# Optimization experiments

Hardware: AMD Instinct MI355X
Metric: run time of the kernel (lower is better)

The kernel has to match this reference:

```python
import jax, jax.numpy as jnp
import numpy as np

T = 0.2


def _cdist(a, b):
    # Euclidean cdist with zero-safe sqrt (grad 0 at coincident points, like torch)
    d2 = (a * a).sum(-1)[:, None] + (b * b).sum(-1)[None, :] - 2.0 * (a @ b.T)
    d2 = jnp.maximum(d2, 0.0)
    safe = jnp.where(d2 > 0, d2, 1.0)
    return jnp.where(d2 > 0, jnp.sqrt(safe), 0.0)


def _generator(eps, W_in, b_in, W_blk, b_blk, W_out, b_out):
    x = eps @ W_in.T + b_in
    for i in range(W_blk.shape[0]):  # 4 residual MLP blocks
        x = x + jax.nn.relu(x @ W_blk[i].T + b_blk[i])
    return x @ W_out.T + b_out


def setup_inputs() -> dict:
    N, D, H = 4096, 128, 512
    key = jax.random.key(0)
    ks = jax.random.split(key, 16)

    def lin(kw, kb, fan_in, shape_w, shape_b):
        bound = 1.0 / np.sqrt(fan_in)
        W = jax.random.uniform(kw, shape_w, jnp.float32, -bound, bound)
        b = jax.random.uniform(kb, shape_b, jnp.float32, -bound, bound)
        return W, b

    W_in, b_in = lin(ks[0], ks[1], D, (H, D), (H,))
    W_blk, b_blk = lin(ks[2], ks[3], H, (4, H, H), (4, H))
    W_out, b_out = lin(ks[4], ks[5], H, (D, H), (D,))
    y_pos = jax.random.normal(ks[6], (N, D), jnp.float32)
    eps = jax.random.normal(ks[7], (N, D), jnp.float32)
    return {"y_pos": y_pos, "eps": eps, "W_in": W_in, "b_in": b_in,
            "W_blk": W_blk, "b_blk": b_blk, "W_out": W_out, "b_out": b_out}


def reference(y_pos, eps, W_in, b_in, W_blk, b_blk, W_out, b_out):
    x = _generator(eps, W_in, b_in, W_blk, b_blk, W_out, b_out)  # [N, D]
    N = y_pos.shape[0]
    dist_pos = _cdist(x, y_pos)                                   # [N, N]
    dist_neg = _cdist(x, x) + jnp.eye(x.shape[0], dtype=x.dtype) * 1e6
    A = jnp.concatenate([-dist_pos / T, -dist_neg / T], axis=-1)  # [N, 2N]
    A_row = jax.nn.softmax(A, axis=-1)
    A_col = jax.nn.softmax(A, axis=-2)
    A_soft = jnp.sqrt(A_row * A_col)
    A_pos = A_soft[:, :N]
    A_neg = A_soft[:, N:]
    s_pos = A_pos.sum(axis=1, keepdims=True)
    s_neg = A_neg.sum(axis=1, keepdims=True)
    Wpos = A_pos * s_neg
    # torch in-place: Wpos *= s_neg mutates A_pos BEFORE A_pos.sum is taken,
    # so Wneg = A_neg * (A_pos * s_neg).sum(1) = A_neg * s_pos * s_neg
    Wneg = A_neg * (s_pos * s_neg)
    V = Wpos @ y_pos - Wneg @ x                                   # drifting field
    target = jax.lax.stop_gradient(x + V)
    return jnp.mean((x - target) ** 2)
```

## Files before the change

kernel.cpp:

```cpp
#include <hip/hip_runtime.h>
#include <math.h>

#define N 4096
#define D 128
#define H 512
#define KSPLIT 4
#define SC_LOG2 7.2134752044f

typedef short bf16x8 __attribute__((ext_vector_type(8)));
typedef float f32x4 __attribute__((ext_vector_type(4)));
typedef unsigned short u16x8 __attribute__((ext_vector_type(8)));
typedef unsigned short u16;
typedef _Float16 f16;
typedef _Float16 f16x4 __attribute__((ext_vector_type(4)));

#define MFMA(a, b, c) __builtin_amdgcn_mfma_f32_16x16x32_bf16((a), (b), (c), 0, 0, 0)

__device__ __forceinline__ float fexp2(float x)
{
#if __has_builtin(__builtin_amdgcn_exp2f)
    return __builtin_amdgcn_exp2f(x);
#else
    return exp2f(x);
#endif
}

__device__ __forceinline__ float fsqrt(float x)
{
#if __has_builtin(__builtin_amdgcn_sqrtf)
    return __builtin_amdgcn_sqrtf(x);
#else
    return sqrtf(x);
#endif
}

__device__ __forceinline__ float bf2f(u16 h)
{
    return __uint_as_float(((unsigned)h) << 16);
}

__device__ __forceinline__ u16 rtn_bf16(float v)
{
    unsigned u = __float_as_uint(v);
    return (u16)((u + 0x7FFFu + ((u >> 16) & 1u)) >> 16);
}

__device__ __forceinline__ void split1(float v, u16& h, u16& l)
{
    u16 hh = rtn_bf16(v);
    float r = v - bf2f(hh);
    h = hh;
    l = rtn_bf16(r);
}

__device__ __forceinline__ void split1_trunc(float v, u16& h, u16& l)
{
    unsigned bv = __float_as_uint(v);
    unsigned hb = bv & 0xFFFF0000u;
    float r = v - __uint_as_float(hb);
    h = (u16)(hb >> 16);
    l = (u16)(__float_as_uint(r) >> 16);
}

template <int CTRL>
__device__ __forceinline__ float dppf(float x)
{
    int r = __builtin_amdgcn_update_dpp(0, __float_as_int(x), CTRL, 0xF, 0xF, true);
    return __int_as_float(r);
}

struct SplitDesc { const float* src; u16* h; int n; };
struct SplitArgs { SplitDesc d[4]; };

__global__ __launch_bounds__(256) void split_multi(SplitArgs args)
{
    SplitDesc de = args.d[blockIdx.y];
    int idx = (blockIdx.x * 256 + threadIdx.x) * 4;
    if (idx >= de.n) return;
    float4 v = *(const float4*)(de.src + idx);
    ushort4 hv;
    hv.x = rtn_bf16(v.x); hv.y = rtn_bf16(v.y);
    hv.z = rtn_bf16(v.z); hv.w = rtn_bf16(v.w);
    *(ushort4*)(de.h + idx) = hv;
}

__global__ __launch_bounds__(512) void gen_fused(
    const float* __restrict__ eps,
    const u16* __restrict__ Win, const u16* __restrict__ Wblk,
    const u16* __restrict__ Wout,
    const float* __restrict__ b_in, const float* __restrict__ b_blk,
    const float* __restrict__ b_out,
    float* __restrict__ xo, u16* __restrict__ xh)
{
    __shared__ u16 XhS[16][520], XlS[16][520];
    const int t = threadIdx.x;
    const int w = t >> 6, lane = t & 63;
    const int quad = lane >> 4, l16 = lane & 15;
    const int bm = blockIdx.x * 16;

    {
        int idx = t * 4;
        int row = idx >> 7, col = idx & 127;
        float4 v = *(const float4*)(eps + (size_t)(bm + row) * D + col);
        ushort4 hv, lv;
        split1(v.x, hv.x, lv.x); split1(v.y, hv.y, lv.y);
        split1(v.z, hv.z, lv.z); split1(v.w, hv.w, lv.w);
        *(ushort4*)&XhS[row][col] = hv;
        *(ushort4*)&XlS[row][col] = lv;
    }
    __syncthreads();

    auto layer = [&](const u16* __restrict__ W, const float* __restrict__ bias,
                     int K, bool rr) {
        const int nb = w * 64;
        f32x4 acc[4] = {};
        const int NT = K >> 5;
        bf16x8 bh[4], bn[4];
        #pragma unroll
        for (int ni = 0; ni < 4; ++ni)
            bh[ni] = *(const bf16x8*)(W + (size_t)(nb + ni * 16 + l16) * K + quad * 8);
        for (int kt = 0; kt < NT; ++kt) {
            const int kk = kt * 32 + quad * 8;
            bf16x8 af  = *(const bf16x8*)&XhS[l16][kk];
            bf16x8 alf = *(const bf16x8*)&XlS[l16][kk];
            if (kt + 1 < NT) {
                #pragma unroll
                for (int ni = 0; ni < 4; ++ni)
                    bn[ni] = *(const bf16x8*)
                        (W + (size_t)(nb + ni * 16 + l16) * K + kk + 32);
            }
            #pragma unroll
            for (int ni = 0; ni < 4; ++ni) {
                acc[ni] = MFMA(af,  bh[ni], acc[ni]);
                acc[ni] = MFMA(alf, bh[ni], acc[ni]);
            }
            if (kt + 1 < NT) {
                #pragma unroll
                for (int ni = 0; ni < 4; ++ni) bh[ni] = bn[ni];
            }
        }
        float bl4[4];
        #pragma unroll
        for (int ni = 0; ni < 4; ++ni) bl4[ni] = bias[nb + ni * 16 + l16];
        __syncthreads();
        #pragma unroll
        for (int ni = 0; ni < 4; ++ni) {
            const int col = nb + ni * 16 + l16;
            #pragma unroll
            for (int r = 0; r < 4; ++r) {
                const int row = quad * 4 + r;
                float v = acc[ni][r] + bl4[ni];
                if (rr) {
                    float prev = bf2f(XhS[row][col]) + bf2f(XlS[row][col]);
                    v = prev + fmaxf(v, 0.0f);
                }
                u16 hh, ll;
                split1_trunc(v, hh, ll);
                XhS[row][col] = hh;
                XlS[row][col] = ll;
            }
        }
        __syncthreads();
    };

    layer(Win, b_in, D, false);
    for (int i = 0; i < 4; ++i)
        layer(Wblk + (size_t)i * H * H, b_blk + i * H, H, true);

    {
        const int n0 = w * 16;
        f32x4 acc5 = {};
        const int NT = H >> 5;
        bf16x8 bh5 = *(const bf16x8*)(Wout + (size_t)(n0 + l16) * H + quad * 8);
        for (int kt = 0; kt < NT; ++kt) {
            const int kk = kt * 32 + quad * 8;
            bf16x8 af  = *(const bf16x8*)&XhS[l16][kk];
            bf16x8 alf = *(const bf16x8*)&XlS[l16][kk];
            bf16x8 bn5;
            if (kt + 1 < NT)
                bn5 = *(const bf16x8*)(Wout + (size_t)(n0 + l16) * H + kk + 32);
            acc5 = MFMA(af,  bh5, acc5);
            acc5 = MFMA(alf, bh5, acc5);
            if (kt + 1 < NT) bh5 = bn5;
        }
        const int col = n0 + l16;
        const float bl = b_out[col];
        #pragma unroll
        for (int r = 0; r < 4; ++r) {
            const int gm = bm + quad * 4 + r;
            float v = acc5[r] + bl;
            xo[(size_t)gm * D + col] = v;
            xh[(size_t)gm * D + col] = rtn_bf16(v);
        }
    }
}

__global__ __launch_bounds__(256) void rownorm(
    const float* __restrict__ X, const float* __restrict__ Y,
    float* __restrict__ nx, float* __restrict__ ny)
{
    const float* src = blockIdx.y ? Y : X;
    float* dst = blockIdx.y ? ny : nx;
    const int t = threadIdx.x;
    const int row = blockIdx.x * 64 + (t >> 2);
    const int q = t & 3;
    const float* rp = src + (size_t)row * D + q * 32;
    float s = 0.f;
    #pragma unroll
    for (int i = 0; i < 8; ++i) {
        float4 v = *(const float4*)(rp + i * 4);
        s += v.x * v.x + v.y * v.y + v.z * v.z + v.w * v.w;
    }
    s += __shfl_xor(s, 1);
    s += __shfl_xor(s, 2);
    if (q == 0) dst[row] = s;
}

__global__ __launch_bounds__(256) void transpose_rtn(
    const float* __restrict__ X, const float* __restrict__ Y,
    u16* __restrict__ Xth, u16* __restrict__ Yth)
{
    const float* src = blockIdx.z ? Y : X;
    u16* th = blockIdx.z ? Yth : Xth;
    __shared__ float tile[32][33];
    const int t = threadIdx.x;
    const int r0 = blockIdx.x * 32, c0 = blockIdx.y * 32;
    {
        int rit = t >> 3, coff = (t & 7) * 4;
        float4 v = *(const float4*)(src + (size_t)(r0 + rit) * D + c0 + coff);
        tile[rit][coff + 0] = v.x; tile[rit][coff + 1] = v.y;
        tile[rit][coff + 2] = v.z; tile[rit][coff + 3] = v.w;
    }
    __syncthreads();
    {
        int cit = t >> 3, roff = (t & 7) * 4;
        ushort4 hv;
        hv.x = rtn_bf16(tile[roff + 0][cit]);
        hv.y = rtn_bf16(tile[roff + 1][cit]);
        hv.z = rtn_bf16(tile[roff + 2][cit]);
        hv.w = rtn_bf16(tile[roff + 3][cit]);
        *(ushort4*)(th + (size_t)(c0 + cit) * N + r0 + roff) = hv;
    }
}

__global__ __launch_bounds__(256) void dist_fused(
    const u16* __restrict__ Xh, const u16* __restrict__ Yh,
    const float* __restrict__ nx, const float* __restrict__ ny,
    f16* __restrict__ Apos, f16* __restrict__ Aneg,
    float* __restrict__ prm_p, float* __restrict__ prs_p,
    float* __restrict__ pcm_p, float* __restrict__ pcs_p,
    float* __restrict__ prm_n, float* __restrict__ prs_n)
{
    const int mat = blockIdx.z;
    const u16* Bhp = mat ? Xh : Yh;
    const float* nb = mat ? nx : ny;
    f16* Out = mat ? Aneg : Apos;
    float* prm = mat ? prm_n : prm_p;
    float* prs = mat ? prs_n : prs_p;

    __shared__ u16 XhS[128][40], YhS[128][40];
    const int t = threadIdx.x;
    const int w = t >> 6, lane = t & 63;
    const int quad = lane >> 4, l16 = lane & 15;
    const int bm = blockIdx.y * 128, bn = blockIdx.x * 128;
    f32x4 acc[2][8] = {};

    for (int k0 = 0; k0 < D; k0 += 32) {
        __syncthreads();
        #pragma unroll
        for (int p = 0; p < 2; ++p) {
            int slot = t + p * 256;
            int row = slot >> 2, koff = (slot & 3) << 3;
            *(u16x8*)&XhS[row][koff] =
                *(const u16x8*)(Xh + (size_t)(bm + row) * D + k0 + koff);
        }
        #pragma unroll
        for (int p = 0; p < 2; ++p) {
            int slot = t + p * 256;
            int row = slot >> 2, koff = (slot & 3) << 3;
            int pr = ((row & 3) << 4) | ((row & 63) >> 2) | (row & 64);
            int kf = koff ^ (((pr >> 4) & 3) << 3);
            *(u16x8*)&YhS[pr][kf] =
                *(const u16x8*)(Bhp + (size_t)(bn + row) * D + k0 + koff);
        }
        __syncthreads();
        bf16x8 af[2], bhf[8];
        #pragma unroll
        for (int mi = 0; mi < 2; ++mi)
            af[mi] = *(const bf16x8*)&XhS[w * 32 + mi * 16 + l16][quad * 8];
        #pragma unroll
        for (int ni = 0; ni < 8; ++ni) {
            int nn = ni & 3, hf = ni >> 2;
            bhf[ni] = *(const bf16x8*)
                &YhS[hf * 64 + nn * 16 + l16][(quad * 8) ^ (nn << 3)];
        }
        #pragma unroll
        for (int mi = 0; mi < 2; ++mi)
            #pragma unroll
            for (int ni = 0; ni < 8; ++ni)
                acc[mi][ni] = MFMA(af[mi], bhf[ni], acc[mi][ni]);
    }
    const int jb = bn + (l16 << 2);
    const float SC2 = SC_LOG2 * SC_LOG2;
    const float c2 = -2.0f * SC2;
    const float4 n0v = *(const float4*)(nb + jb);
    const float4 n1v = *(const float4*)(nb + jb + 64);
    const float nl[8] = {n0v.x * SC2, n0v.y * SC2, n0v.z * SC2, n0v.w * SC2,
                         n1v.x * SC2, n1v.y * SC2, n1v.z * SC2, n1v.w * SC2};
    #pragma unroll
    for (int mi = 0; mi < 2; ++mi)
        #pragma unroll
        for (int r = 0; r < 4; ++r) {
            const int gm = bm + w * 32 + mi * 16 + quad * 4 + r;
            const float nxm = nx[gm] * SC2;
            f16x4 ov0, ov1;
            #pragma unroll
            for (int nn = 0; nn < 4; ++nn) {
                float s0 = fsqrt(fmaxf(
                    fmaf(acc[mi][nn][r], c2, nxm + nl[nn]), 0.f));
                float s1 = fsqrt(fmaxf(
                    fmaf(acc[mi][4 + nn][r], c2, nxm + nl[4 + nn]), 0.f));
                if (mat) {
                    if (gm == jb + nn) s0 = 5.0e6f;
                    if (gm == jb + 64 + nn) s1 = 5.0e6f;
                }
                acc[mi][nn][r] = s0;
                acc[mi][4 + nn][r] = s1;
                ov0[nn] = (f16)(-s0);
                ov1[nn] = (f16)(-s1);
            }
            *(f16x4*)(Out + (size_t)gm * N + jb) = ov0;
            *(f16x4*)(Out + (size_t)gm * N + jb + 64) = ov1;
        }
    float m[2][4];
    #pragma unroll
    for (int mi = 0; mi < 2; ++mi)
        #pragma unroll
        for (int r = 0; r < 4; ++r) {
            float v = fminf(fminf(fminf(acc[mi][0][r], acc[mi][1][r]),
                                  fminf(acc[mi][2][r], acc[mi][3][r])),
                            fminf(fminf(acc[mi][4][r], acc[mi][5][r]),
                                  fminf(acc[mi][6][r], acc[mi][7][r])));
            v = fminf(v, dppf<0xB1>(v));
            v = fminf(v, dppf<0x4E>(v));
            v = fminf(v, dppf<0x141>(v));
            v = fminf(v, dppf<0x140>(v));
            m[mi][r] = v;
        }
    float mn = fminf(fminf(fminf(m[0][0], m[0][1]), fminf(m[0][2], m[0][3])),
                     fminf(fminf(m[1][0], m[1][1]), fminf(m[1][2], m[1][3])));
    mn = fminf(mn, __shfl_xor(mn, 16));
    mn = fminf(mn, __shfl_xor(mn, 32));
    float sig[2][4] = {};
    float cs[8] = {};
    #pragma unroll
    for (int mi = 0; mi < 2; ++mi)
        #pragma unroll
        for (int ni = 0; ni < 8; ++ni) {
            float e0 = fexp2(mn - acc[mi][ni][0]);
            float e1 = fexp2(mn - acc[mi][ni][1]);
            float e2 = fexp2(mn - acc[mi][ni][2]);
            float e3 = fexp2(mn - acc[mi][ni][3]);
            sig[mi][0] += e0; sig[mi][1] += e1;
            sig[mi][2] += e2; sig[mi][3] += e3;
            cs[ni] += (e0 + e1) + (e2 + e3);
        }
    const int ct = blockIdx.x;
    #pragma unroll
    for (int mi = 0; mi < 2; ++mi)
        #pragma unroll
        for (int r = 0; r < 4; ++r) {
            float s = sig[mi][r];
            s += dppf<0xB1>(s);
            s += dppf<0x4E>(s);
            s += dppf<0x141>(s);
            s += dppf<0x140>(s);
            s *= fexp2(m[mi][r] - mn);
            if (l16 == 0) {
                int grow = bm + w * 32 + mi * 16 + quad * 4 + r;
                prm[(size_t)ct * N + grow] = -m[mi][r];
                prs[(size_t)ct * N + grow] = s;
            }
        }
    if (mat == 0) {
        const int rt = blockIdx.y * 4 + w;
        #pragma unroll
        for (int ni = 0; ni < 8; ++ni) {
            cs[ni] += __shfl_xor(cs[ni], 16);
            cs[ni] += __shfl_xor(cs[ni], 32);
        }
        if (quad == 0) {
            float4 c0 = {cs[0], cs[1], cs[2], cs[3]};
            float4 c1 = {cs[4], cs[5], cs[6], cs[7]};
            float4 m4 = {-mn, -mn, -mn, -mn};
            *(float4*)(pcs_p + (size_t)rt * N + jb) = c0;
            *(float4*)(pcs_p + (size_t)rt * N + jb + 64) = c1;
            *(float4*)(pcm_p + (size_t)rt * N + jb) = m4;
            *(float4*)(pcm_p + (size_t)rt * N + jb + 64) = m4;
        }
    }
}

__global__ __launch_bounds__(256) void stats_combine(
    const float* __restrict__ prm_p, const float* __restrict__ prs_p,
    const float* __restrict__ prm_n, const float* __restrict__ prs_n,
    const float* __restrict__ pcm_p, const float* __restrict__ pcs_p,
    float* __restrict__ m_row, float* __restrict__ isr,
    float* __restrict__ m_col, float* __restrict__ isc)
{
    __shared__ float Ms[4][64], Ss[4][64];
    const int t = threadIdx.x;
    const int g = t >> 6, l = t & 63;
    const int idx = blockIdx.x * 64 + l;

    float m = -3.0e38f, s = 0.f;
    if (idx < N) {
        const int i = idx;
        const int c0 = g * 8;
        #pragma unroll 4
        for (int c = c0; c < c0 + 8; ++c) {
            m = fmaxf(m, prm_p[(size_t)c * N + i]);
            m = fmaxf(m, prm_n[(size_t)c * N + i]);
        }
        #pragma unroll 4
        for (int c = c0; c < c0 + 8; ++c) {
            s += prs_p[(size_t)c * N + i] * fexp2(prm_p[(size_t)c * N + i] - m);
            s += prs_n[(size_t)c * N + i] * fexp2(prm_n[(size_t)c * N + i] - m);
        }
    } else {
        const int mat = (idx - N) >> 12;
        const int j = idx & (N - 1);
        const float* pm = mat ? prm_n : pcm_p;
        const float* ps = mat ? prs_n : pcs_p;
        const int cnt = mat ? 8 : 32;
        const int cb = g * cnt;
        #pragma unroll 4
        for (int c = cb; c < cb + cnt; ++c)
            m = fmaxf(m, pm[(size_t)c * N + j]);
        #pragma unroll 4
        for (int c = cb; c < cb + cnt; ++c)
            s += ps[(size_t)c * N + j] * fexp2(pm[(size_t)c * N + j] - m);
    }
    Ms[g][l] = m; Ss[g][l] = s;
    __syncthreads();
    if (g == 0) {
        float m0 = Ms[0][l], m1 = Ms[1][l], m2 = Ms[2][l], m3 = Ms[3][l];
        float mm = fmaxf(fmaxf(m0, m1), fmaxf(m2, m3));
        float ss = Ss[0][l] * fexp2(m0 - mm) + Ss[1][l] * fexp2(m1 - mm)
                 + Ss[2][l] * fexp2(m2 - mm) + Ss[3][l] * fexp2(m3 - mm);
        if (idx < N) {
            m_row[idx] = mm;
            isr[idx] = 1.0f / sqrtf(ss);
        } else {
            const int mat = (idx - N) >> 12;
            const int j = idx & (N - 1);
            m_col[mat * N + j] = mm;
            isc[mat * N + j] = 1.0f / sqrtf(ss);
        }
    }
}

__global__ __launch_bounds__(256) void pv_mfma(
    const f16* __restrict__ Apos, const f16* __restrict__ Aneg,
    const u16* __restrict__ Yth, const u16* __restrict__ Xth,
    const float* __restrict__ m_row, const float* __restrict__ isr,
    const float* __restrict__ m_col, const float* __restrict__ isc,
    float* __restrict__ u_part, float* __restrict__ w_part,
    float* __restrict__ sp_part, float* __restrict__ sn_part)
{
    const int mat = blockIdx.z;
    const f16* Am = mat ? Aneg : Apos;
    const u16* Bh = mat ? Xth : Yth;
    const float* mc = m_col + mat * N;
    const float* ic = isc + mat * N;
    float* Cp = (mat ? w_part : u_part) + (size_t)blockIdx.y * (N * D);
    float* spn = (mat ? sn_part : sp_part) + (size_t)blockIdx.y * N;

    __shared__ u16 BhS[128][72];
    __shared__ u16 PhS[64][72], PlS[64][72];
    __shared__ float mrS[64], isrS[64];

    const int t = threadIdx.x;
    const int w = t >> 6, lane = t & 63;
    const int quad = lane >> 4, l16 = lane & 15;
    const int bm = blockIdx.x * 64;
    const int jbase = blockIdx.y * (N / KSPLIT);
    const int arow = t >> 4;
    const int aj = (t & 15) << 2;

    if (t < 64) { mrS[t] = m_row[bm + t]; isrS[t] = isr[bm + t]; }

    f32x4 acc[8] = {};
    float rs[4] = {0.f, 0.f, 0.f, 0.f};

    for (int jt = 0; jt < (N / KSPLIT) / 64; ++jt) {
        const int j0 = jbase + jt * 64;
        __syncthreads();
        #pragma unroll
        for (int p = 0; p < 4; ++p) {
            int slot = t + p * 256;
            int d = slot >> 3, joff = (slot & 7) << 3;
            *(u16x8*)&BhS[d][joff] = *(const u16x8*)(Bh + (size_t)d * N + j0 + joff);
        }
        float4 mcv = *(const float4*)(mc + j0 + aj);
        float4 icv = *(const float4*)(ic + j0 + aj);
        #pragma unroll
        for (int s = 0; s < 4; ++s) {
            int row = arow + s * 16;
            f16x4 av = *(const f16x4*)(Am + (size_t)(bm + row) * N + j0 + aj);
            float mr = mrS[row], sr = isrS[row];
            float p0 = fexp2((float)av.x - 0.5f * (mr + mcv.x)) * (sr * icv.x);
            float p1 = fexp2((float)av.y - 0.5f * (mr + mcv.y)) * (sr * icv.y);
            float p2 = fexp2((float)av.z - 0.5f * (mr + mcv.z)) * (sr * icv.z);
            float p3 = fexp2((float)av.w - 0.5f * (mr + mcv.w)) * (sr * icv.w);
            rs[s] += p0 + p1 + p2 + p3;
            ushort4 hv, lv;
            split1_trunc(p0, hv.x, lv.x); split1_trunc(p1, hv.y, lv.y);
            split1_trunc(p2, hv.z, lv.z); split1_trunc(p3, hv.w, lv.w);
            *(ushort4*)&PhS[row][aj] = hv;
            *(ushort4*)&PlS[row][aj] = lv;
        }
        __syncthreads();
        #pragma unroll
        for (int ks = 0; ks < 2; ++ks) {
            const int kk = ks * 32 + quad * 8;
            bf16x8 ph = *(const bf16x8*)&PhS[w * 16 + l16][kk];
            bf16x8 pl = *(const bf16x8*)&PlS[w * 16 + l16][kk];
            #pragma unroll
            for (int ni = 0; ni < 8; ++ni) {
                bf16x8 bh = *(const bf16x8*)&BhS[ni * 16 + l16][kk];
                acc[ni] = MFMA(ph, bh, acc[ni]);
                acc[ni] = MFMA(pl, bh, acc[ni]);
            }
        }
    }
    #pragma unroll
    for (int ni = 0; ni < 8; ++ni)
        #pragma unroll
        for (int r = 0; r < 4; ++r) {
            int row = w * 16 + quad * 4 + r;
            int col = ni * 16 + l16;
            Cp[(size_t)(bm + row) * D + col] = acc[ni][r];
        }
    #pragma unroll
    for (int s = 0; s < 4; ++s) {
        float v = rs[s];
        v += __shfl_xor(v, 1); v += __shfl_xor(v, 2);
        v += __shfl_xor(v, 4); v += __shfl_xor(v, 8);
        if (l16 == 0) spn[bm + arow + s * 16] = v;
    }
}

__global__ __launch_bounds__(256) void final_reduce(const float* __restrict__ u_part,
    const float* __restrict__ w_part, const float* __restrict__ sp_part,
    const float* __restrict__ sn_part, double* __restrict__ acc_part)
{
    __shared__ float red[256];
    const int t = threadIdx.x;
    const int idx = blockIdx.x * 256 + t;
    float u = 0.f, w = 0.f;
    #pragma unroll
    for (int c = 0; c < KSPLIT; ++c) {
        u += u_part[(size_t)c * (N * D) + idx];
        w += w_part[(size_t)c * (N * D) + idx];
    }
    const int i = idx >> 7;
    float sp = 0.f, sn = 0.f;
    #pragma unroll
    for (int c = 0; c < KSPLIT; ++c) {
        sp += sp_part[(size_t)c * N + i];
        sn += sn_part[(size_t)c * N + i];
    }
    const float v = sn * u - sp * sn * w;
    red[t] = v * v; __syncthreads();
    for (int s = 128; s > 0; s >>= 1) { if (t < s) red[t] += red[t + s]; __syncthreads(); }
    if (!t) acc_part[blockIdx.x] = (double)red[0];
}

__global__ __launch_bounds__(256) void finalize(const double* __restrict__ acc_part,
                                                float* __restrict__ out)
{
    __shared__ double red[256];
    const int t = threadIdx.x;
    double s = 0.0;
    #pragma unroll
    for (int i = 0; i < 8; ++i) s += acc_part[t + i * 256];
    red[t] = s; __syncthreads();
    for (int st = 128; st > 0; st >>= 1) {
        if (t < st) red[t] += red[t + st];
        __syncthreads();
    }
    if (!t) out[0] = (float)(red[0] * (1.0 / ((double)N * (double)D)));
}

extern "C" void kernel_launch(void* const* d_in, const int* in_sizes, int n_in,
                              void* d_out, int out_size, void* d_ws, size_t ws_size,
                              hipStream_t stream)
{
    const float* y_pos = (const float*)d_in[0];
    const float* eps   = (const float*)d_in[1];
    const float* W_in  = (const float*)d_in[2];
    const float* b_in  = (const float*)d_in[3];
    const float* W_blk = (const float*)d_in[4];
    const float* b_blk = (const float*)d_in[5];
    const float* W_out = (const float*)d_in[6];
    const float* b_out = (const float*)d_in[7];
    float* out = (float*)d_out;
    (void)in_sizes; (void)n_in; (void)out_size; (void)ws_size;

    char* p = (char*)d_ws;
    auto alloc = [&](size_t bytes) {
        char* r = p;
        p += (bytes + 255) & ~(size_t)255;
        return r;
    };
    double* acc_part = (double*)alloc(2048 * 8);
    float* sp_part = (float*)alloc((size_t)KSPLIT * N * 4);
    float* sn_part = (float*)alloc((size_t)KSPLIT * N * 4);
    float* m_row  = (float*)alloc(N * 4);
    float* isr    = (float*)alloc(N * 4);
    float* m_col  = (float*)alloc(2 * N * 4);
    float* isc    = (float*)alloc(2 * N * 4);
    float* nx     = (float*)alloc(N * 4);
    float* ny     = (float*)alloc(N * 4);
    float* xo  = (float*)alloc((size_t)N * D * 4);
    u16* xh    = (u16*)alloc((size_t)N * D * 2);
    u16* xth   = (u16*)alloc((size_t)N * D * 2);
    u16* yh    = (u16*)alloc((size_t)N * D * 2);
    u16* yth   = (u16*)alloc((size_t)N * D * 2);
    char* genreg = alloc((size_t)KSPLIT * N * D * 4 * 2);
    u16* wih = (u16*)genreg;
    u16* wbh = wih + (size_t)H * D;
    u16* woh = wbh + (size_t)4 * H * H;
    float* prm_p = (float*)genreg;
    float* prs_p = prm_p + 32 * N;
    float* prm_n = prs_p + 32 * N;
    float* prs_n = prm_n + 32 * N;
    float* pcm_p = prs_n + 32 * N;
    float* pcs_p = pcm_p + 128 * N;
    float* u_part = (float*)genreg;
    float* w_part = u_part + (size_t)KSPLIT * N * D;
    f16* Apos = (f16*)alloc((size_t)N * N * 2);
    f16* Aneg = (f16*)alloc((size_t)N * N * 2);

    SplitArgs sa;
    sa.d[0] = { y_pos, yh,  N * D };
    sa.d[1] = { W_in,  wih, H * D };
    sa.d[2] = { W_blk, wbh, 4 * H * H };
    sa.d[3] = { W_out, woh, D * H };
    split_multi<<<dim3(1024, 4), 256, 0, stream>>>(sa);

    gen_fused<<<N / 16, 512, 0, stream>>>(eps, wih, wbh, woh,
                                          b_in, b_blk, b_out, xo, xh);

    rownorm<<<dim3(N / 64, 2), 256, 0, stream>>>(xo, y_pos, nx, ny);

    transpose_rtn<<<dim3(N / 32, D / 32, 2), 256, 0, stream>>>(
        xo, y_pos, xth, yth);

    dist_fused<<<dim3(N / 128, N / 128, 2), 256, 0, stream>>>(
        xh, yh, nx, ny, Apos, Aneg,
        prm_p, prs_p, pcm_p, pcs_p, prm_n, prs_n);

    stats_combine<<<192, 256, 0, stream>>>(prm_p, prs_p, prm_n, prs_n,
                                           pcm_p, pcs_p,
                                           m_row, isr, m_col, isc);

    pv_mfma<<<dim3(N / 64, KSPLIT, 2), 256, 0, stream>>>(Apos, Aneg,
        yth, xth, m_row, isr, m_col, isc, u_part, w_part, sp_part, sn_part);

    final_reduce<<<(N * D) / 256, 256, 0, stream>>>(u_part, w_part,
                                                    sp_part, sn_part, acc_part);
    finalize<<<1, 256, 0, stream>>>(acc_part, out);
}
```

Measured before the change: 228.9 us.

## Stage generator weights through LDS with double-buffered direct global-to-LDS loads

The generator MLP kernel now streams each weight K-slice into shared memory with global_load_lds double buffering, instead of each wave loading its own weight fragments into registers. The next slice is prefetched while MFMAs consume the current one, and the k loops are fully unrolled. This aims to hide global load latency and cut register pressure. In exchange it adds a block-wide barrier per k-step and about 64KB of extra LDS, which may limit occupancy.

Measured after the change: 270.9 us. 18.4% more time.

```diff
diff --git a/kernel.cpp b/kernel.cpp
--- a/kernel.cpp
+++ b/kernel.cpp
@@ -15,6 +15,9 @@
 typedef _Float16 f16x4 __attribute__((ext_vector_type(4)));
 
 #define MFMA(a, b, c) __builtin_amdgcn_mfma_f32_16x16x32_bf16((a), (b), (c), 0, 0, 0)
+
+using gvoid = const __attribute__((address_space(1))) void;
+using lvoid = __attribute__((address_space(3))) void;
 
 __device__ __forceinline__ float fexp2(float x)
 {
@@ -84,6 +87,73 @@
     *(ushort4*)(de.h + idx) = hv;
 }
 
+template <int ROWS>
+__device__ __forceinline__ void stage_w(const u16* __restrict__ W, int K, int kt,
+                                        u16* ws, int t)
+{
+    constexpr int ISS = ROWS / 128;
+    #pragma unroll
+    for (int p = 0; p < ISS; ++p) {
+        const int slot = t + p * 512;
+        const int c = slot & (ROWS - 1);
+        const int q = slot / ROWS;
+        const u16* g = W + (size_t)c * K + kt * 32 + q * 8;
+        __builtin_amdgcn_global_load_lds((gvoid*)g,
+                                         (lvoid*)(ws + (size_t)slot * 8),
+                                         16, 0, 0);
+    }
+}
+
+template <int K, bool RR>
+__device__ __forceinline__ void gen_layer(
+    u16 (&XhS)[16][520], u16 (&XlS)[16][520],
+    u16* WS0, u16* WS1,
+    const u16* __restrict__ W, const float* __restrict__ bias,
+    int w, int quad, int l16, int t)
+{
+    const int nb = w * 64;
+    constexpr int NT = K >> 5;
+    f32x4 acc[4] = {};
+    float bl4[4];
+    #pragma unroll
+    for (int ni = 0; ni < 4; ++ni) bl4[ni] = bias[nb + ni * 16 + l16];
+    #pragma unroll
+    for (int kt = 0; kt < NT; ++kt) {
+        u16* cur = (kt & 1) ? WS1 : WS0;
+        u16* nxt = (kt & 1) ? WS0 : WS1;
+        if (kt + 1 < NT) stage_w<512>(W, K, kt + 1, nxt, t);
+        const int kk = kt * 32 + quad * 8;
+        bf16x8 af  = *(const bf16x8*)&XhS[l16][kk];
+        bf16x8 alf = *(const bf16x8*)&XlS[l16][kk];
+        #pragma unroll
+        for (int ni = 0; ni < 4; ++ni) {
+            bf16x8 bh = *(const bf16x8*)
+                (cur + (size_t)(quad * 512 + nb + ni * 16 + l16) * 8);
+            acc[ni] = MFMA(af,  bh, acc[ni]);
+            acc[ni] = MFMA(alf, bh, acc[ni]);
+        }
+        __syncthreads();
+    }
+    #pragma unroll
+    for (int ni = 0; ni < 4; ++ni) {
+        const int col = nb + ni * 16 + l16;
+        #pragma unroll
+        for (int r = 0; r < 4; ++r) {
+            const int row = quad * 4 + r;
+            float v = acc[ni][r] + bl4[ni];
+            if (RR) {
+                float prev = bf2f(XhS[row][col]) + bf2f(XlS[row][col]);
+                v = prev + fmaxf(v, 0.0f);
+            }
+            u16 hh, ll;
+            split1_trunc(v, hh, ll);
+            XhS[row][col] = hh;
+            XlS[row][col] = ll;
+        }
+    }
+    __syncthreads();
+}
+
 __global__ __launch_bounds__(512) void gen_fused(
     const float* __restrict__ eps,
     const u16* __restrict__ Win, const u16* __restrict__ Wblk,
@@ -93,11 +163,13 @@
     float* __restrict__ xo, u16* __restrict__ xh)
 {
     __shared__ u16 XhS[16][520], XlS[16][520];
+    __shared__ u16 WS0[2048 * 8], WS1[2048 * 8];
     const int t = threadIdx.x;
     const int w = t >> 6, lane = t & 63;
     const int quad = lane >> 4, l16 = lane & 15;
     const int bm = blockIdx.x * 16;
 
+    stage_w<512>(Win, D, 0, WS0, t);
     {
         int idx = t * 4;
         int row = idx >> 7, col = idx & 127;
@@ -110,81 +182,38 @@
     }
     __syncthreads();
 
-    auto layer = [&](const u16* __restrict__ W, const float* __restrict__ bias,
-                     int K, bool rr) {
-        const int nb = w * 64;
-        f32x4 acc[4] = {};
-        const int NT = K >> 5;
-        bf16x8 bh[4], bn[4];
-        #pragma unroll
-        for (int ni = 0; ni < 4; ++ni)
-            bh[ni] = *(const bf16x8*)(W + (size_t)(nb + ni * 16 + l16) * K + quad * 8);
+    gen_layer<D, false>(XhS, XlS, WS0, WS1, Win, b_in, w, quad, l16, t);
+    #pragma unroll 1
+    for (int i = 0; i < 4; ++i) {
+        const u16* Wl = Wblk + (size_t)i * H * H;
+        stage_w<512>(Wl, H, 0, WS0, t);
+        __syncthreads();
+        gen_layer<H, true>(XhS, XlS, WS0, WS1, Wl, b_blk + i * H,
+                           w, quad, l16, t);
+    }
+
+    {
+        const int n0 = w * 16;
+        constexpr int NT = H >> 5;
+        f32x4 acc5 = {};
+        const float bl = b_out[n0 + l16];
+        stage_w<128>(Wout, H, 0, WS0, t);
+        __syncthreads();
+        #pragma unroll
         for (int kt = 0; kt < NT; ++kt) {
+            u16* cur = (kt & 1) ? WS1 : WS0;
+            u16* nxt = (kt & 1) ? WS0 : WS1;
+            if (kt + 1 < NT) stage_w<128>(Wout, H, kt + 1, nxt, t);
             const int kk = kt * 32 + quad * 8;
             bf16x8 af  = *(const bf16x8*)&XhS[l16][kk];
             bf16x8 alf = *(const bf16x8*)&XlS[l16][kk];
-            if (kt + 1 < NT) {
-                #pragma unroll
-                for (int ni = 0; ni < 4; ++ni)
-                    bn[ni] = *(const bf16x8*)
-                        (W + (size_t)(nb + ni * 16 + l16) * K + kk + 32);
-            }
-            #pragma unroll
-            for (int ni = 0; ni < 4; ++ni) {
-                acc[ni] = MFMA(af,  bh[ni], acc[ni]);
-                acc[ni] = MFMA(alf, bh[ni], acc[ni]);
-            }
-            if (kt + 1 < NT) {
-                #pragma unroll
-                for (int ni = 0; ni < 4; ++ni) bh[ni] = bn[ni];
-            }
-        }
-        float bl4[4];
-        #pragma unroll
-        for (int ni = 0; ni < 4; ++ni) bl4[ni] = bias[nb + ni * 16 + l16];
-        __syncthreads();
-        #pragma unroll
-        for (int ni = 0; ni < 4; ++ni) {
-            const int col = nb + ni * 16 + l16;
-            #pragma unroll
-            for (int r = 0; r < 4; ++r) {
-                const int row = quad * 4 + r;
-                float v = acc[ni][r] + bl4[ni];
-                if (rr) {
-                    float prev = bf2f(XhS[row][col]) + bf2f(XlS[row][col]);
-                    v = prev + fmaxf(v, 0.0f);
-                }
-                u16 hh, ll;
-                split1_trunc(v, hh, ll);
-                XhS[row][col] = hh;
-                XlS[row][col] = ll;
-            }
-        }
-        __syncthreads();
-    };
-
-    layer(Win, b_in, D, false);
-    for (int i = 0; i < 4; ++i)
-        layer(Wblk + (size_t)i * H * H, b_blk + i * H, H, true);
-
-    {
-        const int n0 = w * 16;
-        f32x4 acc5 = {};
-        const int NT = H >> 5;
-        bf16x8 bh5 = *(const bf16x8*)(Wout + (size_t)(n0 + l16) * H + quad * 8);
-        for (int kt = 0; kt < NT; ++kt) {
-            const int kk = kt * 32 + quad * 8;
-            bf16x8 af  = *(const bf16x8*)&XhS[l16][kk];
-            bf16x8 alf = *(const bf16x8*)&XlS[l16][kk];
-            bf16x8 bn5;
-            if (kt + 1 < NT)
-                bn5 = *(const bf16x8*)(Wout + (size_t)(n0 + l16) * H + kk + 32);
-            acc5 = MFMA(af,  bh5, acc5);
-            acc5 = MFMA(alf, bh5, acc5);
-            if (kt + 1 < NT) bh5 = bn5;
+            bf16x8 bh = *(const bf16x8*)
+                (cur + (size_t)(quad * 128 + n0 + l16) * 8);
+            acc5 = MFMA(af,  bh, acc5);
+            acc5 = MFMA(alf, bh, acc5);
+            __syncthreads();
         }
         const int col = n0 + l16;
-        const float bl = b_out[col];
         #pragma unroll
         for (int r = 0; r < 4; ++r) {
             const int gm = bm + quad * 4 + r;
```
